# Performance work log

Hardware: AMD Instinct MI355X
Metric: run time of the kernel (lower is better)

## Reference

```python
import jax, jax.numpy as jnp
import numpy as np

E = 1024   # embed_dim
H = 16     # head_size
DH = E // H  # head_dim = 64
B, S = 2, 2048
SCALE = 1.0 / np.sqrt(E)  # original divides by sqrt(query.size(-1)) == sqrt(embed_dim)


def setup_inputs() -> dict:
    key = jax.random.key(0)
    ks = jax.random.split(key, 11)
    init = 0.02
    return {
        "query": jax.random.normal(ks[0], (B, S, E), dtype=jnp.float32),
        "key":   jax.random.normal(ks[1], (B, S, E), dtype=jnp.float32),
        "value": jax.random.normal(ks[2], (B, S, E), dtype=jnp.float32),
        # per-head projection weights, stacked over heads: [H, E, DH]
        "Wq": jax.random.normal(ks[3], (H, E, DH), dtype=jnp.float32) * init,
        "bq": jax.random.normal(ks[4], (H, DH), dtype=jnp.float32) * init,
        "Wk": jax.random.normal(ks[5], (H, E, DH), dtype=jnp.float32) * init,
        "bk": jax.random.normal(ks[6], (H, DH), dtype=jnp.float32) * init,
        "Wv": jax.random.normal(ks[7], (H, E, DH), dtype=jnp.float32) * init,
        "bv": jax.random.normal(ks[8], (H, DH), dtype=jnp.float32) * init,
        "Wo": jax.random.normal(ks[9], (E, E), dtype=jnp.float32) * init,
        "bo": jax.random.normal(ks[10], (E,), dtype=jnp.float32) * init,
    }


def reference(query, key, value, Wq, bq, Wk, bk, Wv, bv, Wo, bo):
    # per-head linear projections (vectorized over heads)
    q = jnp.einsum('bse,hed->bhsd', query, Wq) + bq[None, :, None, :]
    k = jnp.einsum('bse,hed->bhsd', key,   Wk) + bk[None, :, None, :]
    v = jnp.einsum('bse,hed->bhsd', value, Wv) + bv[None, :, None, :]
    # NOTE: original code scales by sqrt(embed_dim), not sqrt(head_dim)
    scores = jnp.einsum('bhqd,bhkd->bhqk', q, k) * SCALE
    weights = jax.nn.softmax(scores, axis=-1)
    out = jnp.einsum('bhqk,bhkd->bhqd', weights, v)  # [B,H,S,DH]
    # concat heads along last dim (head order == stacking order)
    out = out.transpose(0, 2, 1, 3).reshape(B, S, H * DH)
    return out @ Wo + bo
```

## Files before the change

### kernel.cpp

```cpp
#include <hip/hip_runtime.h>

typedef __bf16 bf16;
typedef __bf16 bf16x8 __attribute__((ext_vector_type(8)));
typedef __bf16 bf16x4 __attribute__((ext_vector_type(4)));
typedef float f32x4 __attribute__((ext_vector_type(4)));

#define MM 4096
#define NN 1024
#define KK 1024

__device__ __forceinline__ void gload_lds16(const void* g, void* l) {
  __builtin_amdgcn_global_load_lds(
      (const __attribute__((address_space(1))) void*)g,
      (__attribute__((address_space(3))) void*)l, 16, 0, 0);
}

__global__ __launch_bounds__(256) void cvt_x(const float* __restrict__ q,
                                             const float* __restrict__ k,
                                             const float* __restrict__ v,
                                             bf16* __restrict__ out)
{
  int p = blockIdx.y;
  const float* src = (p == 0) ? q : (p == 1 ? k : v);
  bf16* dst = out + (size_t)p * (MM * (size_t)KK);
  int i = (blockIdx.x * 256 + threadIdx.x) * 4;
  float4 val = *(const float4*)(src + i);
  bf16x4 o;
  o.x = (bf16)val.x; o.y = (bf16)val.y; o.z = (bf16)val.z; o.w = (bf16)val.w;
  *(bf16x4*)(dst + i) = o;
}

__global__ __launch_bounds__(256) void cvt_w(const float* __restrict__ Wq,
                                             const float* __restrict__ Wk,
                                             const float* __restrict__ Wv,
                                             const float* __restrict__ Wo,
                                             bf16* __restrict__ Wt,
                                             bf16* __restrict__ Wot)
{
  __shared__ bf16 Sl[64 * 72];
  const int t = threadIdx.x;
  const int bid = blockIdx.x;
  const int p = bid >> 8, t8 = bid & 255;
  const int ti = t >> 4, c4 = (t & 15) * 4;

  if (p < 3) {
    const float* W = (p == 0) ? Wq : (p == 1 ? Wk : Wv);
    const int h = t8 >> 4, e0 = (t8 & 15) << 6;
#pragma unroll
    for (int r = 0; r < 4; ++r) {
      int e_l = r * 16 + ti;
      float4 val = *(const float4*)(W + (h << 16) + (e0 + e_l) * 64 + c4);
      bf16x4 o; o.x = (bf16)val.x; o.y = (bf16)val.y; o.z = (bf16)val.z; o.w = (bf16)val.w;
      *(bf16x4*)(Sl + e_l * 72 + c4) = o;
    }
    __syncthreads();
#pragma unroll
    for (int r = 0; r < 4; ++r) {
      int d_l = r * 16 + ti;
      bf16x4 o;
      o.x = Sl[(c4 + 0) * 72 + d_l];
      o.y = Sl[(c4 + 1) * 72 + d_l];
      o.z = Sl[(c4 + 2) * 72 + d_l];
      o.w = Sl[(c4 + 3) * 72 + d_l];
      *(bf16x4*)(Wt + (size_t)p * 1048576 + (size_t)((h << 6) + d_l) * 1024 + e0 + c4) = o;
    }
  } else {
    const int n0 = (t8 >> 4) << 6, k0 = (t8 & 15) << 6;
#pragma unroll
    for (int r = 0; r < 4; ++r) {
      int k_l = r * 16 + ti;
      float4 val = *(const float4*)(Wo + (size_t)(k0 + k_l) * 1024 + n0 + c4);
      bf16x4 o; o.x = (bf16)val.x; o.y = (bf16)val.y; o.z = (bf16)val.z; o.w = (bf16)val.w;
      *(bf16x4*)(Sl + k_l * 72 + c4) = o;
    }
    __syncthreads();
#pragma unroll
    for (int r = 0; r < 4; ++r) {
      int n_l = r * 16 + ti;
      bf16x4 o;
      o.x = Sl[(c4 + 0) * 72 + n_l];
      o.y = Sl[(c4 + 1) * 72 + n_l];
      o.z = Sl[(c4 + 2) * 72 + n_l];
      o.w = Sl[(c4 + 3) * 72 + n_l];
      *(bf16x4*)(Wot + (size_t)(n0 + n_l) * 1024 + k0 + c4) = o;
    }
  }
}

__device__ __forceinline__ void gemm_body(const bf16* __restrict__ A,
                                          const bf16* __restrict__ Bt,
                                          bf16* As, bf16* Bs,
                                          int m0, int n0, f32x4 (&acc)[4][4])
{
  const int tid = threadIdx.x;
  const int w = tid >> 6, L = tid & 63;
  const int quad = L >> 4, l16 = L & 15;
  const int wm = (w & 1) << 6, wn = (w >> 1) << 6;

  const bf16* Ag = A + (size_t)(m0 + w * 32 + (L >> 2)) * KK + (L & 3) * 8;
  const bf16* Bg = Bt + (size_t)(n0 + w * 32 + (L >> 2)) * KK + (L & 3) * 8;
  bf16* Al = As + w * 1024;
  bf16* Bl = Bs + w * 1024;

  for (int kt = 0; kt < KK / 32; ++kt) {
    __syncthreads();
    const bf16* a0 = Ag + kt * 32;
    const bf16* b0 = Bg + kt * 32;
    gload_lds16(a0, Al);
    gload_lds16(a0 + 16 * KK, Al + 512);
    gload_lds16(b0, Bl);
    gload_lds16(b0 + 16 * KK, Bl + 512);
    __syncthreads();
    bf16x8 af[4], bfr[4];
#pragma unroll
    for (int mi = 0; mi < 4; ++mi)
      af[mi] = *(const bf16x8*)(As + (wm + mi * 16 + l16) * 32 + quad * 8);
#pragma unroll
    for (int ni = 0; ni < 4; ++ni)
      bfr[ni] = *(const bf16x8*)(Bs + (wn + ni * 16 + l16) * 32 + quad * 8);
#pragma unroll
    for (int mi = 0; mi < 4; ++mi)
#pragma unroll
      for (int ni = 0; ni < 4; ++ni)
        acc[mi][ni] = __builtin_amdgcn_mfma_f32_16x16x32_bf16(af[mi], bfr[ni],
                                                              acc[mi][ni], 0, 0, 0);
  }
}

__global__ __launch_bounds__(256) void gemm_proj(const bf16* __restrict__ X,
                                                 const bf16* __restrict__ Wt,
                                                 const float* __restrict__ b0,
                                                 const float* __restrict__ b1,
                                                 const float* __restrict__ b2,
                                                 bf16* __restrict__ Out)
{
  __shared__ bf16 As[4096], Bs[4096];
  int p = blockIdx.y;
  const bf16* A = X + (size_t)p * 4194304;
  const bf16* Bt = Wt + (size_t)p * 1048576;
  const float* bias = (p == 0) ? b0 : (p == 1 ? b1 : b2);
  bf16* C = Out + (size_t)p * 4194304;
  int bx = blockIdx.x;
  int m0 = (bx >> 3) << 7, n0 = (bx & 7) << 7;
  f32x4 acc[4][4] = {};
  gemm_body(A, Bt, As, Bs, m0, n0, acc);
  const int L = threadIdx.x & 63, w = threadIdx.x >> 6;
  const int quad = L >> 4, l16 = L & 15;
  const int wm = (w & 1) << 6, wn = (w >> 1) << 6;
#pragma unroll
  for (int ni = 0; ni < 4; ++ni) {
    int col = n0 + wn + ni * 16 + l16;
    float bv = bias[col];
#pragma unroll
    for (int mi = 0; mi < 4; ++mi)
#pragma unroll
      for (int r = 0; r < 4; ++r) {
        int row = m0 + wm + mi * 16 + quad * 4 + r;
        C[(size_t)row * NN + col] = (bf16)(acc[mi][ni][r] + bv);
      }
  }
}

__global__ __launch_bounds__(256) void gemm_outp(const bf16* __restrict__ A,
                                                 const bf16* __restrict__ Bt,
                                                 const float* __restrict__ bias,
                                                 float* __restrict__ C)
{
  __shared__ bf16 As[4096], Bs[4096];
  int bx = blockIdx.x;
  int m0 = (bx >> 3) << 7, n0 = (bx & 7) << 7;
  f32x4 acc[4][4] = {};
  gemm_body(A, Bt, As, Bs, m0, n0, acc);
  const int L = threadIdx.x & 63, w = threadIdx.x >> 6;
  const int quad = L >> 4, l16 = L & 15;
  const int wm = (w & 1) << 6, wn = (w >> 1) << 6;
#pragma unroll
  for (int ni = 0; ni < 4; ++ni) {
    int col = n0 + wn + ni * 16 + l16;
    float bv = bias[col];
#pragma unroll
    for (int mi = 0; mi < 4; ++mi)
#pragma unroll
      for (int r = 0; r < 4; ++r) {
        int row = m0 + wm + mi * 16 + quad * 4 + r;
        C[(size_t)row * NN + col] = acc[mi][ni][r] + bv;
      }
  }
}

__global__ __launch_bounds__(256) void flash_attn(const bf16* __restrict__ Qm,
                                                  const bf16* __restrict__ Km,
                                                  const bf16* __restrict__ Vm,
                                                  bf16* __restrict__ Om)
{
  __shared__ bf16 Kl[64 * 72];
  __shared__ bf16 Vt[64 * 72];
  __shared__ bf16 Pl[4][16 * 72];
  const int tid = threadIdx.x;
  const int w = tid >> 6, L = tid & 63;
  const int quad = L >> 4, l16 = L & 15;
  const int qb = blockIdx.x & 31;
  const int bh = blockIdx.x >> 5;
  const int b = bh >> 4, h = bh & 15;
  const int s0 = qb << 6;
  const size_t base = (size_t)b * 2048 * 1024 + h * 64;

  const bf16* qp = Qm + base + (size_t)(s0 + w * 16 + l16) * 1024 + quad * 8;
  bf16x8 qf0 = *(const bf16x8*)qp;
  bf16x8 qf1 = *(const bf16x8*)(qp + 32);
  const float SL = 0.03125f * 1.44269504088896f;
#pragma unroll
  for (int j = 0; j < 8; ++j) {
    qf0[j] = (bf16)((float)qf0[j] * SL);
    qf1[j] = (bf16)((float)qf1[j] * SL);
  }

  float l_i[4] = {0.f, 0.f, 0.f, 0.f};
  f32x4 oacc[4] = {};

  const int kcol = ((L & 15) << 2) | (L >> 4);
  const bf16* Kg = Km + base + (size_t)L * 1024 + w * 16;
  const bf16* Vg = Vm + base + (size_t)L * 1024 + w * 16;

  bf16x8 k0 = *(const bf16x8*)Kg;
  bf16x8 k1 = *(const bf16x8*)(Kg + 8);
  bf16x8 v0 = *(const bf16x8*)Vg;
  bf16x8 v1 = *(const bf16x8*)(Vg + 8);

  for (int kt = 0; kt < 32; ++kt) {
    __syncthreads();
    *(bf16x8*)(Kl + L * 72 + w * 16) = k0;
    *(bf16x8*)(Kl + L * 72 + w * 16 + 8) = k1;
#pragma unroll
    for (int j = 0; j < 8; ++j) {
      Vt[(w * 16 + j) * 72 + kcol] = v0[j];
      Vt[(w * 16 + 8 + j) * 72 + kcol] = v1[j];
    }
    if (kt + 1 < 32) {
      const bf16* kg = Kg + (size_t)(kt + 1) * 65536;
      const bf16* vg = Vg + (size_t)(kt + 1) * 65536;
      k0 = *(const bf16x8*)kg;
      k1 = *(const bf16x8*)(kg + 8);
      v0 = *(const bf16x8*)vg;
      v1 = *(const bf16x8*)(vg + 8);
    }
    __syncthreads();

    f32x4 sacc[4];
#pragma unroll
    for (int ns = 0; ns < 4; ++ns) {
      bf16x8 kf0 = *(const bf16x8*)(Kl + (ns * 16 + l16) * 72 + quad * 8);
      bf16x8 kf1 = *(const bf16x8*)(Kl + (ns * 16 + l16) * 72 + 32 + quad * 8);
      f32x4 s = {0.f, 0.f, 0.f, 0.f};
      s = __builtin_amdgcn_mfma_f32_16x16x32_bf16(qf0, kf0, s, 0, 0, 0);
      s = __builtin_amdgcn_mfma_f32_16x16x32_bf16(qf1, kf1, s, 0, 0, 0);
      sacc[ns] = s;
    }

#pragma unroll
    for (int r = 0; r < 4; ++r) {
      float p0 = exp2f(sacc[0][r]);
      float p1 = exp2f(sacc[1][r]);
      float p2 = exp2f(sacc[2][r]);
      float p3 = exp2f(sacc[3][r]);
      l_i[r] += (p0 + p1) + (p2 + p3);
      bf16x4 pv;
      pv.x = (bf16)p0; pv.y = (bf16)p1; pv.z = (bf16)p2; pv.w = (bf16)p3;
      *(bf16x4*)(&Pl[w][(quad * 4 + r) * 72 + l16 * 4]) = pv;
    }
    asm volatile("s_waitcnt lgkmcnt(0)" ::: "memory");
    bf16x8 pf0 = *(const bf16x8*)(&Pl[w][l16 * 72 + quad * 8]);
    bf16x8 pf1 = *(const bf16x8*)(&Pl[w][l16 * 72 + 32 + quad * 8]);
#pragma unroll
    for (int ds = 0; ds < 4; ++ds) {
      bf16x8 vf0 = *(const bf16x8*)(Vt + (ds * 16 + l16) * 72 + quad * 8);
      bf16x8 vf1 = *(const bf16x8*)(Vt + (ds * 16 + l16) * 72 + 32 + quad * 8);
      oacc[ds] = __builtin_amdgcn_mfma_f32_16x16x32_bf16(pf0, vf0, oacc[ds], 0, 0, 0);
      oacc[ds] = __builtin_amdgcn_mfma_f32_16x16x32_bf16(pf1, vf1, oacc[ds], 0, 0, 0);
    }
  }

#pragma unroll
  for (int r = 0; r < 4; ++r) {
    float l = l_i[r];
    l += __shfl_xor(l, 1);
    l += __shfl_xor(l, 2);
    l += __shfl_xor(l, 4);
    l += __shfl_xor(l, 8);
    float inv = 1.f / l;
    bf16* op = Om + base + (size_t)(s0 + w * 16 + quad * 4 + r) * 1024;
#pragma unroll
    for (int ds = 0; ds < 4; ++ds)
      op[ds * 16 + l16] = (bf16)(oacc[ds][r] * inv);
  }
}

extern "C" void kernel_launch(void* const* d_in, const int* in_sizes, int n_in,
                              void* d_out, int out_size, void* d_ws, size_t ws_size,
                              hipStream_t stream)
{
  const float* q  = (const float*)d_in[0];
  const float* k  = (const float*)d_in[1];
  const float* v  = (const float*)d_in[2];
  const float* Wq = (const float*)d_in[3];
  const float* bq = (const float*)d_in[4];
  const float* Wk = (const float*)d_in[5];
  const float* bk = (const float*)d_in[6];
  const float* Wv = (const float*)d_in[7];
  const float* bv = (const float*)d_in[8];
  const float* Wo = (const float*)d_in[9];
  const float* bo = (const float*)d_in[10];

  char* ws = (char*)d_ws;
  bf16* Xb  = (bf16*)ws;
  bf16* Wt  = (bf16*)(ws + 25165824);
  bf16* Wot = (bf16*)(ws + 31457280);
  bf16* QKV = (bf16*)(ws + 33554432);
  bf16* O   = (bf16*)ws;

  cvt_x<<<dim3(4096, 3), 256, 0, stream>>>(q, k, v, Xb);
  cvt_w<<<dim3(1024), 256, 0, stream>>>(Wq, Wk, Wv, Wo, Wt, Wot);
  gemm_proj<<<dim3(256, 3), 256, 0, stream>>>(Xb, Wt, bq, bk, bv, QKV);
  flash_attn<<<dim3(1024), 256, 0, stream>>>(QKV, QKV + 4194304, QKV + 8388608, O);
  gemm_outp<<<dim3(256), 256, 0, stream>>>(O, Wot, bo, (float*)d_out);
}
```

Measured before the change: 259.8 us.

## Emit V pre-transposed from projection GEMM and split keys across warps in attention

The projection kernel now computes V as Wv^T·X^T, writing V already transposed per head, so attention no longer transposes V through shared memory. Each attention warp now takes all 64 query rows over a quarter of the key range. It loads K and V fragments straight from global memory with no LDS staging or per-tile barriers, then reduces partial outputs and row sums across warps through LDS at the end. This removes the per-tile syncs and the scalar LDS transpose, at the cost of more registers (launch bounds set to 3 blocks), uncoalesced strided stores in the V GEMM epilogue, and an extra cross-warp reduction.

New measurement: 288.9 us. 11.2% more time.

```diff
diff --git a/kernel.cpp b/kernel.cpp
--- a/kernel.cpp
+++ b/kernel.cpp
@@ -3,6 +3,7 @@
 typedef __bf16 bf16;
 typedef __bf16 bf16x8 __attribute__((ext_vector_type(8)));
 typedef __bf16 bf16x4 __attribute__((ext_vector_type(4)));
+typedef __bf16 bf16x2 __attribute__((ext_vector_type(2)));
 typedef float f32x4 __attribute__((ext_vector_type(4)));
 
 #define MM 4096
@@ -127,37 +128,56 @@
   }
 }
 
-__global__ __launch_bounds__(256) void gemm_proj(const bf16* __restrict__ X,
+__global__ __launch_bounds__(256) void gemm_qkvt(const bf16* __restrict__ Xb,
                                                  const bf16* __restrict__ Wt,
-                                                 const float* __restrict__ b0,
-                                                 const float* __restrict__ b1,
-                                                 const float* __restrict__ b2,
-                                                 bf16* __restrict__ Out)
+                                                 const float* __restrict__ bq,
+                                                 const float* __restrict__ bk,
+                                                 const float* __restrict__ bv,
+                                                 bf16* __restrict__ QK,
+                                                 bf16* __restrict__ VtOut)
 {
   __shared__ bf16 As[4096], Bs[4096];
-  int p = blockIdx.y;
-  const bf16* A = X + (size_t)p * 4194304;
-  const bf16* Bt = Wt + (size_t)p * 1048576;
-  const float* bias = (p == 0) ? b0 : (p == 1 ? b1 : b2);
-  bf16* C = Out + (size_t)p * 4194304;
-  int bx = blockIdx.x;
-  int m0 = (bx >> 3) << 7, n0 = (bx & 7) << 7;
-  f32x4 acc[4][4] = {};
-  gemm_body(A, Bt, As, Bs, m0, n0, acc);
+  const int bid = blockIdx.x;
   const int L = threadIdx.x & 63, w = threadIdx.x >> 6;
   const int quad = L >> 4, l16 = L & 15;
   const int wm = (w & 1) << 6, wn = (w >> 1) << 6;
-#pragma unroll
-  for (int ni = 0; ni < 4; ++ni) {
-    int col = n0 + wn + ni * 16 + l16;
-    float bv = bias[col];
-#pragma unroll
-    for (int mi = 0; mi < 4; ++mi)
-#pragma unroll
-      for (int r = 0; r < 4; ++r) {
-        int row = m0 + wm + mi * 16 + quad * 4 + r;
-        C[(size_t)row * NN + col] = (bf16)(acc[mi][ni][r] + bv);
-      }
+  f32x4 acc[4][4] = {};
+
+  if (bid < 512) {
+    const int p = bid >> 8, t8 = bid & 255;
+    const int m0 = (t8 >> 3) << 7, n0 = (t8 & 7) << 7;
+    gemm_body(Xb + (size_t)p * 4194304, Wt + (size_t)p * 1048576, As, Bs, m0, n0, acc);
+    const float* bias = p ? bk : bq;
+    bf16* C = QK + (size_t)p * 4194304;
+#pragma unroll
+    for (int ni = 0; ni < 4; ++ni) {
+      int col = n0 + wn + ni * 16 + l16;
+      float bvv = bias[col];
+#pragma unroll
+      for (int mi = 0; mi < 4; ++mi)
+#pragma unroll
+        for (int r = 0; r < 4; ++r) {
+          int row = m0 + wm + mi * 16 + quad * 4 + r;
+          C[(size_t)row * NN + col] = (bf16)(acc[mi][ni][r] + bvv);
+        }
+    }
+  } else {
+    const int t8 = bid - 512;
+    const int m0 = (t8 >> 5) << 7, n0 = (t8 & 31) << 7;
+    gemm_body(Wt + 2 * 1048576, Xb + 2 * 4194304, As, Bs, m0, n0, acc);
+#pragma unroll
+    for (int ni = 0; ni < 4; ++ni) {
+      int n = n0 + wn + ni * 16 + l16;
+      int bb = n >> 11, sl = n & 2047;
+#pragma unroll
+      for (int mi = 0; mi < 4; ++mi)
+#pragma unroll
+        for (int r = 0; r < 4; ++r) {
+          int m = m0 + wm + mi * 16 + quad * 4 + r;
+          VtOut[(size_t)((bb << 4) + (m >> 6)) * 131072 + (m & 63) * 2048 + sl]
+              = (bf16)(acc[mi][ni][r] + bv[m]);
+        }
+    }
   }
 }
 
@@ -188,14 +208,15 @@
   }
 }
 
-__global__ __launch_bounds__(256) void flash_attn(const bf16* __restrict__ Qm,
-                                                  const bf16* __restrict__ Km,
-                                                  const bf16* __restrict__ Vm,
-                                                  bf16* __restrict__ Om)
-{
-  __shared__ bf16 Kl[64 * 72];
-  __shared__ bf16 Vt[64 * 72];
-  __shared__ bf16 Pl[4][16 * 72];
+__global__ __launch_bounds__(256, 3) void flash_attn(const bf16* __restrict__ Qm,
+                                                     const bf16* __restrict__ Km,
+                                                     const bf16* __restrict__ Vt,
+                                                     bf16* __restrict__ Om)
+{
+  __shared__ bf16 Pl[4][64 * 40];
+  __shared__ float Obuf[2][4096];
+  __shared__ float Lred[4][64];
+
   const int tid = threadIdx.x;
   const int w = tid >> 6, L = tid & 63;
   const int quad = L >> 4, l16 = L & 15;
@@ -203,95 +224,143 @@
   const int bh = blockIdx.x >> 5;
   const int b = bh >> 4, h = bh & 15;
   const int s0 = qb << 6;
-  const size_t base = (size_t)b * 2048 * 1024 + h * 64;
-
-  const bf16* qp = Qm + base + (size_t)(s0 + w * 16 + l16) * 1024 + quad * 8;
-  bf16x8 qf0 = *(const bf16x8*)qp;
-  bf16x8 qf1 = *(const bf16x8*)(qp + 32);
+  const size_t baseQ = (size_t)b * 2097152 + h * 64;
+  const size_t baseV = (size_t)bh * 131072;
+
+  bf16x8 qf[4][2];
   const float SL = 0.03125f * 1.44269504088896f;
-#pragma unroll
-  for (int j = 0; j < 8; ++j) {
-    qf0[j] = (bf16)((float)qf0[j] * SL);
-    qf1[j] = (bf16)((float)qf1[j] * SL);
-  }
-
-  float l_i[4] = {0.f, 0.f, 0.f, 0.f};
-  f32x4 oacc[4] = {};
-
-  const int kcol = ((L & 15) << 2) | (L >> 4);
-  const bf16* Kg = Km + base + (size_t)L * 1024 + w * 16;
-  const bf16* Vg = Vm + base + (size_t)L * 1024 + w * 16;
-
-  bf16x8 k0 = *(const bf16x8*)Kg;
-  bf16x8 k1 = *(const bf16x8*)(Kg + 8);
-  bf16x8 v0 = *(const bf16x8*)Vg;
-  bf16x8 v1 = *(const bf16x8*)(Vg + 8);
-
-  for (int kt = 0; kt < 32; ++kt) {
-    __syncthreads();
-    *(bf16x8*)(Kl + L * 72 + w * 16) = k0;
-    *(bf16x8*)(Kl + L * 72 + w * 16 + 8) = k1;
-#pragma unroll
-    for (int j = 0; j < 8; ++j) {
-      Vt[(w * 16 + j) * 72 + kcol] = v0[j];
-      Vt[(w * 16 + 8 + j) * 72 + kcol] = v1[j];
-    }
-    if (kt + 1 < 32) {
-      const bf16* kg = Kg + (size_t)(kt + 1) * 65536;
-      const bf16* vg = Vg + (size_t)(kt + 1) * 65536;
-      k0 = *(const bf16x8*)kg;
-      k1 = *(const bf16x8*)(kg + 8);
-      v0 = *(const bf16x8*)vg;
-      v1 = *(const bf16x8*)(vg + 8);
-    }
-    __syncthreads();
-
-    f32x4 sacc[4];
-#pragma unroll
-    for (int ns = 0; ns < 4; ++ns) {
-      bf16x8 kf0 = *(const bf16x8*)(Kl + (ns * 16 + l16) * 72 + quad * 8);
-      bf16x8 kf1 = *(const bf16x8*)(Kl + (ns * 16 + l16) * 72 + 32 + quad * 8);
-      f32x4 s = {0.f, 0.f, 0.f, 0.f};
-      s = __builtin_amdgcn_mfma_f32_16x16x32_bf16(qf0, kf0, s, 0, 0, 0);
-      s = __builtin_amdgcn_mfma_f32_16x16x32_bf16(qf1, kf1, s, 0, 0, 0);
-      sacc[ns] = s;
-    }
-
-#pragma unroll
-    for (int r = 0; r < 4; ++r) {
-      float p0 = exp2f(sacc[0][r]);
-      float p1 = exp2f(sacc[1][r]);
-      float p2 = exp2f(sacc[2][r]);
-      float p3 = exp2f(sacc[3][r]);
-      l_i[r] += (p0 + p1) + (p2 + p3);
-      bf16x4 pv;
-      pv.x = (bf16)p0; pv.y = (bf16)p1; pv.z = (bf16)p2; pv.w = (bf16)p3;
-      *(bf16x4*)(&Pl[w][(quad * 4 + r) * 72 + l16 * 4]) = pv;
+  {
+    const bf16* qp = Qm + baseQ + (size_t)(s0 + l16) * 1024 + quad * 8;
+#pragma unroll
+    for (int mi = 0; mi < 4; ++mi)
+#pragma unroll
+      for (int h2 = 0; h2 < 2; ++h2) {
+        bf16x8 t = *(const bf16x8*)(qp + mi * 16384 + h2 * 32);
+#pragma unroll
+        for (int j = 0; j < 8; ++j) t[j] = (bf16)((float)t[j] * SL);
+        qf[mi][h2] = t;
+      }
+  }
+
+  f32x4 oacc[4][4] = {};
+  f32x4 l_i[4] = {};
+
+  const bf16* Kg = Km + baseQ + (size_t)(w * 512 + 2 * l16) * 1024 + quad * 8;
+  const bf16* Vg = Vt + baseV + (size_t)l16 * 2048 + w * 512 + quad * 8;
+  bf16* Pw = &Pl[w][0];
+
+  for (int t = 0; t < 16; ++t) {
+    bf16x8 kf[2][2], vf[4];
+#pragma unroll
+    for (int kt2 = 0; kt2 < 2; ++kt2)
+#pragma unroll
+      for (int h2 = 0; h2 < 2; ++h2)
+        kf[kt2][h2] = *(const bf16x8*)(Kg + kt2 * 1024 + h2 * 32);
+#pragma unroll
+    for (int ds = 0; ds < 4; ++ds)
+      vf[ds] = *(const bf16x8*)(Vg + ds * 32768);
+    Kg += 32768;
+    Vg += 32;
+
+#pragma unroll
+    for (int mi = 0; mi < 4; ++mi) {
+      f32x4 s0f = {0.f, 0.f, 0.f, 0.f}, s1f = {0.f, 0.f, 0.f, 0.f};
+      s0f = __builtin_amdgcn_mfma_f32_16x16x32_bf16(qf[mi][0], kf[0][0], s0f, 0, 0, 0);
+      s0f = __builtin_amdgcn_mfma_f32_16x16x32_bf16(qf[mi][1], kf[0][1], s0f, 0, 0, 0);
+      s1f = __builtin_amdgcn_mfma_f32_16x16x32_bf16(qf[mi][0], kf[1][0], s1f, 0, 0, 0);
+      s1f = __builtin_amdgcn_mfma_f32_16x16x32_bf16(qf[mi][1], kf[1][1], s1f, 0, 0, 0);
+#pragma unroll
+      for (int r = 0; r < 4; ++r) {
+        float p0 = __builtin_amdgcn_exp2f(s0f[r]);
+        float p1 = __builtin_amdgcn_exp2f(s1f[r]);
+        l_i[mi][r] += p0 + p1;
+        bf16x2 pv; pv.x = (bf16)p0; pv.y = (bf16)p1;
+        *(bf16x2*)(Pw + (mi * 16 + quad * 4 + r) * 40 + 2 * l16) = pv;
+      }
     }
     asm volatile("s_waitcnt lgkmcnt(0)" ::: "memory");
-    bf16x8 pf0 = *(const bf16x8*)(&Pl[w][l16 * 72 + quad * 8]);
-    bf16x8 pf1 = *(const bf16x8*)(&Pl[w][l16 * 72 + 32 + quad * 8]);
-#pragma unroll
-    for (int ds = 0; ds < 4; ++ds) {
-      bf16x8 vf0 = *(const bf16x8*)(Vt + (ds * 16 + l16) * 72 + quad * 8);
-      bf16x8 vf1 = *(const bf16x8*)(Vt + (ds * 16 + l16) * 72 + 32 + quad * 8);
-      oacc[ds] = __builtin_amdgcn_mfma_f32_16x16x32_bf16(pf0, vf0, oacc[ds], 0, 0, 0);
-      oacc[ds] = __builtin_amdgcn_mfma_f32_16x16x32_bf16(pf1, vf1, oacc[ds], 0, 0, 0);
-    }
-  }
-
-#pragma unroll
-  for (int r = 0; r < 4; ++r) {
-    float l = l_i[r];
-    l += __shfl_xor(l, 1);
-    l += __shfl_xor(l, 2);
-    l += __shfl_xor(l, 4);
-    l += __shfl_xor(l, 8);
-    float inv = 1.f / l;
-    bf16* op = Om + base + (size_t)(s0 + w * 16 + quad * 4 + r) * 1024;
-#pragma unroll
-    for (int ds = 0; ds < 4; ++ds)
-      op[ds * 16 + l16] = (bf16)(oacc[ds][r] * inv);
+    bf16x8 paf[4];
+#pragma unroll
+    for (int mi = 0; mi < 4; ++mi)
+      paf[mi] = *(const bf16x8*)(Pw + (mi * 16 + l16) * 40 + quad * 8);
+#pragma unroll
+    for (int mi = 0; mi < 4; ++mi)
+#pragma unroll
+      for (int ds = 0; ds < 4; ++ds)
+        oacc[mi][ds] = __builtin_amdgcn_mfma_f32_16x16x32_bf16(paf[mi], vf[ds],
+                                                               oacc[mi][ds], 0, 0, 0);
+  }
+
+#pragma unroll
+  for (int mi = 0; mi < 4; ++mi)
+#pragma unroll
+    for (int r = 0; r < 4; ++r) {
+      float l = l_i[mi][r];
+      l += __shfl_xor(l, 1); l += __shfl_xor(l, 2);
+      l += __shfl_xor(l, 4); l += __shfl_xor(l, 8);
+      l_i[mi][r] = l;
+    }
+  if (l16 == 0) {
+#pragma unroll
+    for (int mi = 0; mi < 4; ++mi)
+#pragma unroll
+      for (int r = 0; r < 4; ++r)
+        Lred[w][mi * 16 + quad * 4 + r] = l_i[mi][r];
+  }
+  if (w >= 2) {
+    f32x4* dst = (f32x4*)&Obuf[w - 2][0];
+#pragma unroll
+    for (int mi = 0; mi < 4; ++mi)
+#pragma unroll
+      for (int ds = 0; ds < 4; ++ds)
+        dst[(mi * 4 + ds) * 64 + L] = oacc[mi][ds];
+  }
+  __syncthreads();
+  if (w < 2) {
+    const f32x4* src = (const f32x4*)&Obuf[w][0];
+#pragma unroll
+    for (int mi = 0; mi < 4; ++mi)
+#pragma unroll
+      for (int ds = 0; ds < 4; ++ds)
+        oacc[mi][ds] += src[(mi * 4 + ds) * 64 + L];
+  }
+  __syncthreads();
+  if (w == 1) {
+    f32x4* dst = (f32x4*)&Obuf[0][0];
+#pragma unroll
+    for (int mi = 0; mi < 2; ++mi)
+#pragma unroll
+      for (int ds = 0; ds < 4; ++ds)
+        dst[(mi * 4 + ds) * 64 + L] = oacc[mi][ds];
+  } else if (w == 0) {
+    f32x4* dst = (f32x4*)&Obuf[1][0];
+#pragma unroll
+    for (int mi = 2; mi < 4; ++mi)
+#pragma unroll
+      for (int ds = 0; ds < 4; ++ds)
+        dst[((mi - 2) * 4 + ds) * 64 + L] = oacc[mi][ds];
+  }
+  __syncthreads();
+  if (w < 2) {
+    const f32x4* src = (const f32x4*)&Obuf[w][0];
+    const int mlo = w * 2;
+#pragma unroll
+    for (int mi2 = 0; mi2 < 2; ++mi2) {
+      const int mi = mlo + mi2;
+#pragma unroll
+      for (int ds = 0; ds < 4; ++ds)
+        oacc[mi][ds] += src[(mi2 * 4 + ds) * 64 + L];
+#pragma unroll
+      for (int r = 0; r < 4; ++r) {
+        int qr = mi * 16 + quad * 4 + r;
+        float lt = Lred[0][qr] + Lred[1][qr] + Lred[2][qr] + Lred[3][qr];
+        float inv = 1.f / lt;
+        bf16* op = Om + baseQ + (size_t)(s0 + qr) * 1024;
+#pragma unroll
+        for (int ds = 0; ds < 4; ++ds)
+          op[ds * 16 + l16] = (bf16)(oacc[mi][ds][r] * inv);
+      }
+    }
   }
 }
 
@@ -315,12 +384,13 @@
   bf16* Xb  = (bf16*)ws;
   bf16* Wt  = (bf16*)(ws + 25165824);
   bf16* Wot = (bf16*)(ws + 31457280);
-  bf16* QKV = (bf16*)(ws + 33554432);
+  bf16* QK  = (bf16*)(ws + 33554432);
+  bf16* Vtg = (bf16*)(ws + 50331648);
   bf16* O   = (bf16*)ws;
 
   cvt_x<<<dim3(4096, 3), 256, 0, stream>>>(q, k, v, Xb);
   cvt_w<<<dim3(1024), 256, 0, stream>>>(Wq, Wk, Wv, Wo, Wt, Wot);
-  gemm_proj<<<dim3(256, 3), 256, 0, stream>>>(Xb, Wt, bq, bk, bv, QKV);
-  flash_attn<<<dim3(1024), 256, 0, stream>>>(QKV, QKV + 4194304, QKV + 8388608, O);
+  gemm_qkvt<<<dim3(768), 256, 0, stream>>>(Xb, Wt, bq, bk, bv, QK, Vtg);
+  flash_attn<<<dim3(1024), 256, 0, stream>>>(QK, QK + 4194304, Vtg, O);
   gemm_outp<<<dim3(256), 256, 0, stream>>>(O, Wot, bo, (float*)d_out);
 }
```
